# Performance work log

Measured on AMD Instinct MI355X. Metric: run time of the kernel, lower is better.

## Reference

```python
import jax, jax.numpy as jnp
import numpy as np
from jax import lax

B0, H0, W0, C0, NH0 = 8, 128, 128, 192, 6
SPLIT = (8, 16)
BN_EPS = 1e-5


def setup_inputs() -> dict:
    key = jax.random.key(0)
    ks = jax.random.split(key, 32)
    r = lambda i, shape, s=0.02: jax.random.normal(ks[i], shape, dtype=jnp.float32) * s
    C, C8 = C0, C0 // 8
    L = H0 * W0
    return dict(
        x=jax.random.normal(ks[0], (B0, L, C), dtype=jnp.float32),
        w_qkv=r(1, (C, 3 * C)), b_qkv=r(2, (3 * C,)),
        w_dw1=r(3, (C, 1, 3, 3), 0.1), b_dw1=r(4, (C,)),
        g_bn1=1.0 + r(5, (C,)), be_bn1=r(6, (C,)),
        w_si1=r(7, (C8, C), 0.05), b_si1=r(8, (C8,)),
        g_si=1.0 + r(9, (C8,)), be_si=r(10, (C8,)),
        w_si2=r(11, (1, C8), 0.05), b_si2=r(12, (1,)),
        w_ci1=r(13, (C8, C), 0.05), b_ci1=r(14, (C8,)),
        g_ci=1.0 + r(15, (C8,)), be_ci=r(16, (C8,)),
        w_ci2=r(17, (C, C8), 0.05), b_ci2=r(18, (C,)),
        w_dw2=r(19, (C, 1, 3, 3), 0.1), b_dw2=r(20, (C,)),
        g_bn2=1.0 + r(21, (C,)), be_bn2=r(22, (C,)),
        w_proj=r(23, (C, C)), b_proj=r(24, (C,)),
        H=H0, W=W0,
    )


def _bn(x, g, b):  # eval-mode BatchNorm2d, running_mean=0, running_var=1, NCHW
    return x * (g / jnp.sqrt(1.0 + BN_EPS))[:, None, None] + b[:, None, None]


def _gelu(x):
    return jax.nn.gelu(x, approximate=False)  # torch nn.GELU default (erf)


def _dwconv3x3(x, w, b):  # x:(B,C,H,W), w:(C,1,3,3) depthwise
    y = lax.conv_general_dilated(x, w, (1, 1), 'SAME',
                                 feature_group_count=x.shape[1],
                                 dimension_numbers=('NCHW', 'OIHW', 'NCHW'))
    return y + b[:, None, None]


def _c1x1(x, w, b):  # 1x1 conv, w:(O,C)
    return jnp.einsum('bchw,oc->bohw', x, w) + b[:, None, None]


def _win_attn(q, k, v, H, W, Hs, Ws, nh):
    # q,k,v: (B, H*W, Cb). qkv1==qkv2==qkv3 in the source (same Linear on same x),
    # so attn1+attn2+attn3 == 3*attn1 and v1+v2+v3 == 3*v1 (faithful math).
    B, L, Cb = q.shape
    hd = Cb // nh
    scale = hd ** (-0.5)
    T = Hs * Ws

    def to_win(t):  # (B,L,Cb) -> (nW, nh, T, hd)
        t = t.reshape(B, H // Hs, Hs, W // Ws, Ws, Cb)
        t = t.transpose(0, 1, 3, 2, 4, 5).reshape(-1, T, nh, hd)
        return t.transpose(0, 2, 1, 3)

    qw, kw, vw = to_win(q), to_win(k), to_win(v)
    attn = jnp.einsum('wntd,wnsd->wnts', qw, kw) * (3.0 * scale)
    attn = jax.nn.softmax(attn, axis=-1)
    out = jnp.einsum('wnts,wnsd->wntd', attn, 3.0 * vw)  # (nW, nh, T, hd)
    out = out.transpose(0, 2, 1, 3).reshape(-1, T, Cb)
    out = out.reshape(B, H // Hs, W // Ws, Hs, Ws, Cb)
    out = out.transpose(0, 1, 3, 2, 4, 5).reshape(B, H, W, Cb)
    return out


def _forward(x, w_qkv, b_qkv, w_dw1, b_dw1, g_bn1, be_bn1,
             w_si1, b_si1, g_si, be_si, w_si2, b_si2,
             w_ci1, b_ci1, g_ci, be_ci, w_ci2, b_ci2,
             w_dw2, b_dw2, g_bn2, be_bn2, w_proj, b_proj, H, W):
    B, L, C = x.shape
    Ch = C // 2
    nh = NH0 // 2

    qkv = (x @ w_qkv + b_qkv).reshape(B, L, 3, C).transpose(2, 0, 1, 3)  # (3,B,L,C)
    mx = max(SPLIT)
    pad_b = (mx - H % mx) % mx
    pad_r = (mx - W % mx) % mx
    qi = qkv.reshape(3 * B, H, W, C)
    qi = jnp.pad(qi, ((0, 0), (0, pad_b), (0, pad_r), (0, 0)))
    _H, _W = H + pad_b, W + pad_r
    qkv = qi.reshape(3, B, _H * _W, C)
    q, k, v = qkv[0], qkv[1], qkv[2]

    fu1 = _win_attn(q[..., :Ch], k[..., :Ch], v[..., :Ch], _H, _W, SPLIT[0], SPLIT[1], nh)
    fu2 = _win_attn(q[..., Ch:], k[..., Ch:], v[..., Ch:], _H, _W, SPLIT[1], SPLIT[0], nh)
    fu = jnp.concatenate([fu1[:, :H, :W, :].reshape(B, L, Ch),
                          fu2[:, :H, :W, :].reshape(B, L, Ch)], axis=-1)

    # NOTE: the source does x.reshape(B,C,L) (a raw reshape, NOT a transpose) -- replicated.
    x_img = x.reshape(B, C, H, W)
    conv_x1 = _gelu(_bn(_dwconv3x3(x_img, w_dw1, b_dw1), g_bn1, be_bn1))

    s = _c1x1(conv_x1, w_si1, b_si1)
    s = _c1x1(_gelu(_bn(s, g_si, be_si)), w_si2, b_si2)   # (B,1,H,W)
    spatial_map = s.reshape(B, L, 1)

    c = conv_x1.mean(axis=(2, 3), keepdims=True)           # AdaptiveAvgPool2d(1)
    c = _c1x1(c, w_ci1, b_ci1)
    c = _c1x1(_gelu(_bn(c, g_ci, be_ci)), w_ci2, b_ci2)    # (B,C,1,1)
    channel_map = c.reshape(B, 1, C)

    fu = fu + fu * jax.nn.sigmoid(spatial_map)
    fu_img = jnp.swapaxes(fu, -2, -1).reshape(B, C, H, W)
    fu_img = _gelu(_bn(_dwconv3x3(fu_img, w_dw2, b_dw2), g_bn2, be_bn2))
    fu = fu_img.transpose(0, 2, 3, 1).reshape(B, L, C)
    fu = fu + fu * jax.nn.sigmoid(channel_map)
    return fu @ w_proj + b_proj


def reference(x, w_qkv, b_qkv, w_dw1, b_dw1, g_bn1, be_bn1,
              w_si1, b_si1, g_si, be_si, w_si2, b_si2,
              w_ci1, b_ci1, g_ci, be_ci, w_ci2, b_ci2,
              w_dw2, b_dw2, g_bn2, be_bn2, w_proj, b_proj, H, W):
    return _forward(x, w_qkv, b_qkv, w_dw1, b_dw1, g_bn1, be_bn1,
                    w_si1, b_si1, g_si, be_si, w_si2, b_si2,
                    w_ci1, b_ci1, g_ci, be_ci, w_ci2, b_ci2,
                    w_dw2, b_dw2, g_bn2, be_bn2, w_proj, b_proj, H, W)
```

## Files before the change

kernel.cpp:

```cpp
#include <hip/hip_runtime.h>

#define Bn 8
#define Hn 128
#define Wn 128
#define Cn 192
#define Ln (Hn*Wn)
#define Mn (Bn*Ln)
#define FUn ((size_t)Mn*Cn)
#define BANKn ((size_t)Mn*96)
#define BN_RSQ 0.9999950000374997f

typedef unsigned short ushort_t;
typedef __attribute__((ext_vector_type(8))) short short8;
typedef __attribute__((ext_vector_type(4))) float f32x4;
typedef __attribute__((ext_vector_type(4))) unsigned int uint4v;

static __device__ __forceinline__ float gelu_f(float x) {
    return 0.5f * x * (1.0f + erff(x * 0.7071067811865475f));
}
static __device__ __forceinline__ float gate1p(float x) {
    return 1.0f + 1.0f / (1.0f + __expf(-x));
}
static __device__ __forceinline__ unsigned short f2bf(float f) {
    unsigned u = __float_as_uint(f);
    return (unsigned short)((u + 0x7FFFu + ((u >> 16) & 1u)) >> 16);
}
static __device__ __forceinline__ unsigned int pk2(float lo, float hi) {
    return (unsigned int)f2bf(lo) | ((unsigned int)f2bf(hi) << 16);
}
static __device__ __forceinline__ float bf2f(ushort_t u) {
    return __uint_as_float((unsigned)u << 16);
}

__global__ __launch_bounds__(256) void qkv_mfma(const ushort_t* __restrict__ Ab,
        const ushort_t* __restrict__ BwT, const float* __restrict__ bias,
        ushort_t* __restrict__ Qp, ushort_t* __restrict__ Kp,
        ushort_t* __restrict__ Vp)
{
    __shared__ __align__(16) ushort_t smem[128 * 64 + 96 * 64];
    ushort_t* As = smem;
    ushort_t* Bs = smem + 128 * 64;
    ushort_t* St = smem;
    ushort_t* Stv = smem;
    const int g1d = blockIdx.x;
    const int rem = g1d % 48;
    const int sib = rem >> 3;
    const int w8 = rem & 7;
    const int wid = (g1d / 48) * 8 + w8;
    const int br = sib & 1;
    const int partp = sib >> 1;
    const int b = wid >> 7, win = wid & 127;
    const int n0g = partp * 192 + br * 96;
    ushort_t* dst = partp == 0 ? Qp : (partp == 1 ? Kp : Vp);
    ushort_t* bptr = dst + (br ? BANKn : 0);
    int hb, wb;
    if (br == 0) { hb = (win >> 3) * 8;  wb = (win & 7) * 16; }
    else         { hb = (win >> 4) * 16; wb = (win & 15) * 8; }
    const int tid = threadIdx.x;
    const int lane = tid & 63;
    const int wrow = (tid >> 6) * 32;
    const int r0 = lane >> 4, cl = lane & 15;
    f32x4 acc[2][6] = {};

    for (int ks = 0; ks < 3; ++ks) {
        const int k0 = ks * 64;
        if (ks) __syncthreads();
        #pragma unroll
        for (int i = 0; i < 2; ++i) {
            int s = tid + i * 256;
            int row = s >> 2, q = s & 3;
            int l = (br == 0) ? (hb + (row >> 4)) * Wn + wb + (row & 15)
                              : (hb + (row >> 3)) * Wn + wb + (row & 7);
            const ushort_t* src = Ab + (size_t)(b * Ln + l) * 192 + k0 + q * 16;
            uint4 u0 = *(const uint4*)(src);
            uint4 u1 = *(const uint4*)(src + 8);
            int r7 = row & 7;
            *(uint4*)&As[row * 64 + (((q * 2) ^ r7) * 8)] = u0;
            *(uint4*)&As[row * 64 + (((q * 2 + 1) ^ r7) * 8)] = u1;
        }
        #pragma unroll
        for (int i = 0; i < 3; ++i) {
            int f = tid + i * 256;
            int col = f % 96, kslot = f / 96;
            uint4 wv = *(const uint4*)(BwT + (size_t)(n0g + col) * 192 + k0 + kslot * 8);
            *(uint4*)&Bs[col * 64 + ((kslot ^ (col & 7)) * 8)] = wv;
        }
        __syncthreads();
        #pragma unroll
        for (int kk = 0; kk < 2; ++kk) {
            int kslot = kk * 4 + r0;
            int ra0 = wrow + cl, ra1 = wrow + 16 + cl;
            short8 a0 = *(const short8*)&As[ra0 * 64 + ((kslot ^ (ra0 & 7)) * 8)];
            short8 a1 = *(const short8*)&As[ra1 * 64 + ((kslot ^ (ra1 & 7)) * 8)];
            #pragma unroll
            for (int n = 0; n < 6; ++n) {
                int col = n * 16 + cl;
                short8 bn = *(const short8*)&Bs[col * 64 + ((kslot ^ (col & 7)) * 8)];
                acc[0][n] = __builtin_amdgcn_mfma_f32_16x16x32_bf16(a0, bn, acc[0][n], 0, 0, 0);
                acc[1][n] = __builtin_amdgcn_mfma_f32_16x16x32_bf16(a1, bn, acc[1][n], 0, 0, 0);
            }
        }
    }
    float bv[6];
    #pragma unroll
    for (int n = 0; n < 6; ++n) bv[n] = bias[n0g + n * 16 + cl];
    __syncthreads();
    const size_t hbase = (size_t)wid * 3;
    if (partp < 2) {
        #pragma unroll
        for (int m = 0; m < 2; ++m)
            #pragma unroll
            for (int n = 0; n < 6; ++n)
                #pragma unroll
                for (int j = 0; j < 4; ++j) {
                    int t = wrow + m * 16 + r0 * 4 + j;
                    St[t * 104 + n * 16 + cl] = f2bf(acc[m][n][j] + bv[n]);
                }
        __syncthreads();
        #pragma unroll
        for (int i = 0; i < 6; ++i) {
            int f = tid + i * 256;
            int ch8 = f & 3, t = (f >> 2) & 127, hd = f >> 9;
            uint4 v = *(const uint4*)&St[t * 104 + hd * 32 + ch8 * 8];
            *(uint4*)(bptr + (hbase + hd) * 4096 + t * 32 + ch8 * 8) = v;
        }
    } else {
        #pragma unroll
        for (int m = 0; m < 2; ++m)
            #pragma unroll
            for (int n = 0; n < 6; ++n)
                #pragma unroll
                for (int j = 0; j < 4; ++j) {
                    int t = wrow + m * 16 + r0 * 4 + j;
                    Stv[(n * 16 + cl) * 136 + t] = f2bf(acc[m][n][j] + bv[n]);
                }
        __syncthreads();
        #pragma unroll
        for (int i = 0; i < 6; ++i) {
            int f = tid + i * 256;
            int t16 = f & 15, ch = (f >> 4) & 31, hd = f >> 9;
            uint4 v = *(const uint4*)&Stv[(hd * 32 + ch) * 136 + t16 * 8];
            *(uint4*)(bptr + (hbase + hd) * 4096 + ch * 128 + t16 * 8) = v;
        }
    }
}

__global__ __launch_bounds__(256) void proj_mfma(const ushort_t* __restrict__ Ab,
        const ushort_t* __restrict__ BwT, const float* __restrict__ bias,
        float* __restrict__ Cout)
{
    __shared__ __align__(16) ushort_t As[128 * 64];
    __shared__ __align__(16) ushort_t Bs[96 * 64];
    const int m0 = blockIdx.x * 128;
    const int n0 = blockIdx.y * 96;
    const int tid = threadIdx.x;
    const int lane = tid & 63;
    const int wrow = (tid >> 6) * 32;
    const int r0 = lane >> 4, cl = lane & 15;
    f32x4 acc[2][6] = {};

    for (int ks = 0; ks < 3; ++ks) {
        const int k0 = ks * 64;
        if (ks) __syncthreads();
        #pragma unroll
        for (int i = 0; i < 2; ++i) {
            int s = tid + i * 256;
            int row = s >> 2, q = s & 3;
            const ushort_t* src = Ab + (size_t)(m0 + row) * 192 + k0 + q * 16;
            uint4 u0 = *(const uint4*)(src);
            uint4 u1 = *(const uint4*)(src + 8);
            int r7 = row & 7;
            *(uint4*)&As[row * 64 + (((q * 2) ^ r7) * 8)] = u0;
            *(uint4*)&As[row * 64 + (((q * 2 + 1) ^ r7) * 8)] = u1;
        }
        #pragma unroll
        for (int i = 0; i < 3; ++i) {
            int f = tid + i * 256;
            int col = f % 96, kslot = f / 96;
            uint4 wv = *(const uint4*)(BwT + (size_t)(n0 + col) * 192 + k0 + kslot * 8);
            *(uint4*)&Bs[col * 64 + ((kslot ^ (col & 7)) * 8)] = wv;
        }
        __syncthreads();
        #pragma unroll
        for (int kk = 0; kk < 2; ++kk) {
            int kslot = kk * 4 + r0;
            int ra0 = wrow + cl, ra1 = wrow + 16 + cl;
            short8 a0 = *(const short8*)&As[ra0 * 64 + ((kslot ^ (ra0 & 7)) * 8)];
            short8 a1 = *(const short8*)&As[ra1 * 64 + ((kslot ^ (ra1 & 7)) * 8)];
            #pragma unroll
            for (int n = 0; n < 6; ++n) {
                int col = n * 16 + cl;
                short8 bn = *(const short8*)&Bs[col * 64 + ((kslot ^ (col & 7)) * 8)];
                acc[0][n] = __builtin_amdgcn_mfma_f32_16x16x32_bf16(a0, bn, acc[0][n], 0, 0, 0);
                acc[1][n] = __builtin_amdgcn_mfma_f32_16x16x32_bf16(a1, bn, acc[1][n], 0, 0, 0);
            }
        }
    }
    #pragma unroll
    for (int m = 0; m < 2; ++m) {
        #pragma unroll
        for (int n = 0; n < 6; ++n) {
            int col = n0 + n * 16 + cl;
            float bv = bias[col];
            #pragma unroll
            for (int j = 0; j < 4; ++j) {
                int row = m0 + wrow + m * 16 + r0 * 4 + j;
                Cout[(size_t)row * 192 + col] = acc[m][n][j] + bv;
            }
        }
    }
}

__global__ __launch_bounds__(256) void attn_mfma(const ushort_t* __restrict__ Qp,
        const ushort_t* __restrict__ Kp, const ushort_t* __restrict__ Vp,
        const float* __restrict__ gate_s, ushort_t* __restrict__ fu_b)
{
    const int widx = threadIdx.x >> 6;
    const int idx = blockIdx.x * 4 + widx;
    const int jhalf = idx & 1;
    const int sub0 = idx >> 1;
    const int branch = (sub0 >= 3072) ? 1 : 0;
    const int sub = sub0 - branch * 3072;
    const int head = sub >> 10;
    const int b = (sub >> 7) & 7;
    const int win = sub & 127;
    const int L = threadIdx.x & 63;
    const int g = L >> 4, q = L & 15;
    int hb, wb;
    if (branch == 0) { hb = (win >> 3) * 8;  wb = (win & 7) * 16; }
    else             { hb = (win >> 4) * 16; wb = (win & 15) * 8; }
    const int cf = branch * 96 + head * 32;
    const int jbase = jhalf * 4;

    const size_t base = (branch ? BANKn : 0)
                      + ((size_t)(b * 128 + win) * 3 + head) * 4096;
    const ushort_t* Qw = Qp + base;
    const ushort_t* Kw = Kp + base;
    const ushort_t* Vw = Vp + base;

    short8 kf[8], qf[4];
    #pragma unroll
    for (int i = 0; i < 8; ++i)
        kf[i] = *(const short8*)(Kw + (16 * i + q) * 32 + 8 * g);
    #pragma unroll
    for (int jj = 0; jj < 4; ++jj)
        qf[jj] = *(const short8*)(Qw + (16 * (jbase + jj) + q) * 32 + 8 * g);
    short8 vf[2][4];
    #pragma unroll
    for (int dblk = 0; dblk < 2; ++dblk)
        #pragma unroll
        for (int s = 0; s < 4; ++s)
            vf[dblk][s] = *(const short8*)(Vw + (16 * dblk + q) * 128 + 32 * s + 8 * g);

    const float SC = 0.5303300858899106f;
    const int src0 = q + ((g & 1) << 5);
    const bool thi = (g >> 1) != 0;
    const bool glo = (g < 2);
    #pragma unroll
    for (int jj = 0; jj < 4; ++jj) {
        const int j = jbase + jj;
        unsigned wA[8], wB[8];
        float ss = 0.0f;
        #pragma unroll
        for (int i = 0; i < 8; ++i) {
            f32x4 z = {};
            f32x4 S = __builtin_amdgcn_mfma_f32_16x16x32_bf16(kf[i], qf[jj], z, 0, 0, 0);
            float p0 = __expf(S[0] * SC), p1 = __expf(S[1] * SC);
            float p2 = __expf(S[2] * SC), p3 = __expf(S[3] * SC);
            ss += (p0 + p1) + (p2 + p3);
            wA[i] = pk2(p0, p1);
            wB[i] = pk2(p2, p3);
        }
        ss += __shfl_xor(ss, 16);
        ss += __shfl_xor(ss, 32);
        int l_own;
        if (branch == 0) l_own = (hb + j) * Wn + wb + q;
        else             l_own = (hb + 2 * j + (q >> 3)) * Wn + wb + (q & 7);
        float s_own = 3.0f * gate_s[(size_t)b * Ln + l_own] / ss;

        f32x4 O0 = {}, O1 = {};
        #pragma unroll
        for (int s = 0; s < 4; ++s) {
            unsigned a0  = (unsigned)__shfl((int)wA[2*s],     src0);
            unsigned b0  = (unsigned)__shfl((int)wB[2*s],     src0);
            unsigned a0h = (unsigned)__shfl((int)wA[2*s],     src0 + 16);
            unsigned b0h = (unsigned)__shfl((int)wB[2*s],     src0 + 16);
            unsigned a1  = (unsigned)__shfl((int)wA[2*s+1],   src0);
            unsigned b1  = (unsigned)__shfl((int)wB[2*s+1],   src0);
            unsigned a1h = (unsigned)__shfl((int)wA[2*s+1],   src0 + 16);
            unsigned b1h = (unsigned)__shfl((int)wB[2*s+1],   src0 + 16);
            uint4v B2u;
            B2u[0] = thi ? a1  : a0;
            B2u[1] = thi ? b1  : b0;
            B2u[2] = thi ? a1h : a0h;
            B2u[3] = thi ? b1h : b0h;
            short8 B2 = *(short8*)&B2u;
            O0 = __builtin_amdgcn_mfma_f32_16x16x32_bf16(vf[0][s], B2, O0, 0, 0, 0);
            O1 = __builtin_amdgcn_mfma_f32_16x16x32_bf16(vf[1][s], B2, O1, 0, 0, 0);
        }
        unsigned w0 = pk2(O0[0] * s_own, O0[1] * s_own);
        unsigned w1 = pk2(O0[2] * s_own, O0[3] * s_own);
        unsigned w2 = pk2(O1[0] * s_own, O1[1] * s_own);
        unsigned w3 = pk2(O1[2] * s_own, O1[3] * s_own);
        unsigned a0 = (unsigned)__shfl((int)w0, src0);
        unsigned a1 = (unsigned)__shfl((int)w1, src0);
        unsigned b0 = (unsigned)__shfl((int)w0, src0 + 16);
        unsigned b1 = (unsigned)__shfl((int)w1, src0 + 16);
        unsigned c0 = (unsigned)__shfl((int)w2, src0);
        unsigned c1 = (unsigned)__shfl((int)w3, src0);
        unsigned d0 = (unsigned)__shfl((int)w2, src0 + 16);
        unsigned d1 = (unsigned)__shfl((int)w3, src0 + 16);
        uint4 o = make_uint4(glo ? a0 : c0, glo ? a1 : c1,
                             glo ? b0 : d0, glo ? b1 : d1);
        *(uint4*)(fu_b + (size_t)(b * Ln + l_own) * 192 + cf + 8 * g) = o;
    }
}

__global__ __launch_bounds__(256) void conv1_k(const float* __restrict__ x,
        const float* __restrict__ wdw, const float* __restrict__ bdw,
        const float* __restrict__ g1, const float* __restrict__ be1,
        const float* __restrict__ w_qkv, const float* __restrict__ w_proj,
        ushort_t* __restrict__ conv1b, ushort_t* __restrict__ xb,
        ushort_t* __restrict__ wqkvT, ushort_t* __restrict__ wprojT,
        float* __restrict__ pooled16)
{
    if (blockIdx.y == 0) {
        int gid = blockIdx.x * 256 + threadIdx.x;
        if (gid < 192 * 576) {
            int k = gid / 576, n = gid - k * 576;
            wqkvT[(size_t)n * 192 + k] = f2bf(w_qkv[gid]);
        } else if (gid < 192 * 576 + 192 * 192) {
            int g2 = gid - 192 * 576;
            int k = g2 / 192, n = g2 - k * 192;
            wprojT[(size_t)n * 192 + k] = f2bf(w_proj[g2]);
        }
    }
    int bc = blockIdx.x;
    int rg = blockIdx.y;
    int c = bc % 192;
    const float* plane = x + (size_t)bc * Ln;
    int t = threadIdx.x;
    int sx = t & 31, sy = t >> 5;
    int w0 = sx * 4, h = rg * 8 + sy;
    float wk[9];
    #pragma unroll
    for (int i = 0; i < 9; ++i) wk[i] = wdw[c * 9 + i];
    float gb = g1[c] * BN_RSQ, bb = be1[c], bd = bdw[c];

    float a[3][6];
    #pragma unroll
    for (int i = 0; i < 3; ++i) {
        int hh = h - 1 + i;
        float4 m = make_float4(0.f, 0.f, 0.f, 0.f);
        if (hh >= 0 && hh < Hn)
            m = *(const float4*)(plane + hh * Wn + w0);
        float lf = __shfl_up(m.w, 1);
        float rt = __shfl_down(m.x, 1);
        a[i][0] = sx ? lf : 0.0f;
        a[i][1] = m.x; a[i][2] = m.y; a[i][3] = m.z; a[i][4] = m.w;
        a[i][5] = (sx < 31) ? rt : 0.0f;
    }
    *(uint2*)(xb + (size_t)bc * Ln + h * Wn + w0) =
        make_uint2(pk2(a[1][1], a[1][2]), pk2(a[1][3], a[1][4]));
    float psum = 0.0f;
    float o[4];
    #pragma unroll
    for (int p = 0; p < 4; ++p) {
        float s = wk[0] * a[0][p];
        s = fmaf(wk[1], a[0][p + 1], s);
        s = fmaf(wk[2], a[0][p + 2], s);
        s = fmaf(wk[3], a[1][p],     s);
        s = fmaf(wk[4], a[1][p + 1], s);
        s = fmaf(wk[5], a[1][p + 2], s);
        s = fmaf(wk[6], a[2][p],     s);
        s = fmaf(wk[7], a[2][p + 1], s);
        s = fmaf(wk[8], a[2][p + 2], s);
        float y = gelu_f((s + bd) * gb + bb);
        psum += y;
        o[p] = y;
    }
    *(uint2*)(conv1b + (size_t)bc * Ln + h * Wn + w0) =
        make_uint2(pk2(o[0], o[1]), pk2(o[2], o[3]));
    __shared__ float red[4];
    for (int off = 32; off; off >>= 1) psum += __shfl_down(psum, off);
    if ((t & 63) == 0) red[t >> 6] = psum;
    __syncthreads();
    if (t == 0)
        pooled16[bc * 16 + rg] = red[0] + red[1] + red[2] + red[3];
}

__global__ __launch_bounds__(192) void gates_k(const ushort_t* __restrict__ conv1b,
        const float* __restrict__ pooled16,
        const float* __restrict__ ws1g, const float* __restrict__ bs1,
        const float* __restrict__ gsi, const float* __restrict__ besi,
        const float* __restrict__ ws2, const float* __restrict__ bs2,
        const float* __restrict__ w1, const float* __restrict__ b1,
        const float* __restrict__ gci, const float* __restrict__ beci,
        const float* __restrict__ w2, const float* __restrict__ b2,
        float* __restrict__ gate_s, float* __restrict__ gate_c)
{
    int blk = blockIdx.x;
    int tid = threadIdx.x;
    if (blk < Bn * Hn) {
        int b = blk >> 7, h = blk & 127;
        __shared__ float ws1T[192 * 24];
        for (int i = tid; i < 192 * 24; i += 192) {
            int c = i / 24, o = i - c * 24;
            ws1T[i] = ws1g[o * 192 + c];
        }
        __syncthreads();
        if (tid < 128) {
            int w = tid;
            float acc24[24] = {};
            const ushort_t* base = conv1b + (size_t)b * 192 * Ln + h * Wn + w;
            #pragma unroll 4
            for (int c = 0; c < 192; ++c) {
                float v = bf2f(base[(size_t)c * Ln]);
                const float4* wp = (const float4*)&ws1T[c * 24];
                #pragma unroll
                for (int o4 = 0; o4 < 6; ++o4) {
                    float4 wv = wp[o4];
                    acc24[o4*4+0] = fmaf(v, wv.x, acc24[o4*4+0]);
                    acc24[o4*4+1] = fmaf(v, wv.y, acc24[o4*4+1]);
                    acc24[o4*4+2] = fmaf(v, wv.z, acc24[o4*4+2]);
                    acc24[o4*4+3] = fmaf(v, wv.w, acc24[o4*4+3]);
                }
            }
            float s2 = bs2[0];
            #pragma unroll
            for (int o = 0; o < 24; ++o)
                s2 = fmaf(gelu_f((acc24[o] + bs1[o]) * (gsi[o] * BN_RSQ) + besi[o]),
                          ws2[o], s2);
            gate_s[(size_t)blk * 128 + w] = gate1p(s2);
        }
    } else {
        int b = blk - Bn * Hn;
        __shared__ float pl[192];
        __shared__ float h1[24];
        int bc = b * 192 + tid;
        float s = 0.0f;
        #pragma unroll
        for (int i = 0; i < 16; ++i) s += pooled16[bc * 16 + i];
        pl[tid] = s * (1.0f / Ln);
        __syncthreads();
        if (tid < 24) {
            float a = b1[tid];
            for (int c = 0; c < 192; ++c) a = fmaf(pl[c], w1[tid * 192 + c], a);
            a = a * (gci[tid] * BN_RSQ) + beci[tid];
            h1[tid] = gelu_f(a);
        }
        __syncthreads();
        float a = b2[tid];
        #pragma unroll
        for (int o = 0; o < 24; ++o) a = fmaf(h1[o], w2[tid * 24 + o], a);
        gate_c[b * 192 + tid] = gate1p(a);
    }
}

__global__ __launch_bounds__(256) void dwconv2_k(const ushort_t* __restrict__ fu_b,
        const float* __restrict__ gate_c,
        const float* __restrict__ wdw, const float* __restrict__ bdw,
        const float* __restrict__ g2, const float* __restrict__ be2,
        ushort_t* __restrict__ out2b)
{
    int bh = blockIdx.x >> 1;
    int whalf = blockIdx.x & 1;
    int b = bh >> 7, h = bh & 127;
    int tid = threadIdx.x;
    __shared__ float cwp[24 * 105];
    for (int idx = tid; idx < 24 * 96; idx += 256) {
        int c8 = idx / 96, r = idx - c8 * 96;
        float v;
        if (r < 72) {
            int i = r / 9, p = r - i * 9;
            v = wdw[(c8 * 8 + i) * 9 + p];
        } else {
            int r2 = r - 72;
            int i = r2 / 3, j = r2 - i * 3;
            int c = c8 * 8 + i;
            float A = g2[c] * BN_RSQ;
            v = (j == 0) ? A : (j == 1) ? fmaf(bdw[c], A, be2[c])
                                        : gate_c[b * 192 + c];
        }
        cwp[c8 * 105 + r] = v;
    }
    __syncthreads();
    const size_t outrow = (size_t)(b * Ln + h * Wn) * 192;
    for (int it = 0; it < 6; ++it) {
        int item = it * 256 + tid;
        int w = whalf * 64 + item / 24;
        int c8 = item % 24;
        int co = c8 * 8;
        const float* wp = &cwp[c8 * 105];
        uint4 nb[3][3];
        #pragma unroll
        for (int r = 0; r < 3; ++r)
            #pragma unroll
            for (int d = 0; d < 3; ++d)
                nb[r][d] = make_uint4(0u, 0u, 0u, 0u);
        #pragma unroll
        for (int r = 0; r < 3; ++r) {
            int hh = h - 1 + r;
            if (hh < 0 || hh >= Hn) continue;
            const ushort_t* rp = fu_b + (size_t)(b * Ln + hh * Wn) * 192 + co;
            #pragma unroll
            for (int d = 0; d < 3; ++d) {
                int w2 = w - 1 + d;
                if (w2 < 0 || w2 >= Wn) continue;
                nb[r][d] = *(const uint4*)(rp + (size_t)w2 * 192);
            }
        }
        unsigned ou[4];
        #pragma unroll
        for (int i = 0; i < 8; ++i) {
            float s = 0.0f;
            #pragma unroll
            for (int r = 0; r < 3; ++r) {
                #pragma unroll
                for (int d = 0; d < 3; ++d) {
                    unsigned word = ((const unsigned*)&nb[r][d])[i >> 1];
                    float v = __uint_as_float((i & 1) ? (word & 0xffff0000u)
                                                      : (word << 16));
                    s = fmaf(wp[i * 9 + r * 3 + d], v, s);
                }
            }
            float A = wp[72 + i * 3];
            float Bc = wp[72 + i * 3 + 1];
            float G = wp[72 + i * 3 + 2];
            float y = gelu_f(fmaf(s, A, Bc)) * G;
            if (i & 1) ou[i >> 1] |= (unsigned)f2bf(y) << 16;
            else       ou[i >> 1] = (unsigned)f2bf(y);
        }
        *(uint4*)(out2b + outrow + (size_t)w * 192 + co) =
            make_uint4(ou[0], ou[1], ou[2], ou[3]);
    }
}

extern "C" void kernel_launch(void* const* d_in, const int* in_sizes, int n_in,
                              void* d_out, int out_size, void* d_ws, size_t ws_size,
                              hipStream_t stream) {
    (void)in_sizes; (void)n_in; (void)out_size; (void)ws_size;
    const float* x      = (const float*)d_in[0];
    const float* w_qkv  = (const float*)d_in[1];
    const float* b_qkv  = (const float*)d_in[2];
    const float* w_dw1  = (const float*)d_in[3];
    const float* b_dw1  = (const float*)d_in[4];
    const float* g_bn1  = (const float*)d_in[5];
    const float* be_bn1 = (const float*)d_in[6];
    const float* w_si1  = (const float*)d_in[7];
    const float* b_si1  = (const float*)d_in[8];
    const float* g_si   = (const float*)d_in[9];
    const float* be_si  = (const float*)d_in[10];
    const float* w_si2  = (const float*)d_in[11];
    const float* b_si2  = (const float*)d_in[12];
    const float* w_ci1  = (const float*)d_in[13];
    const float* b_ci1  = (const float*)d_in[14];
    const float* g_ci   = (const float*)d_in[15];
    const float* be_ci  = (const float*)d_in[16];
    const float* w_ci2  = (const float*)d_in[17];
    const float* b_ci2  = (const float*)d_in[18];
    const float* w_dw2  = (const float*)d_in[19];
    const float* b_dw2  = (const float*)d_in[20];
    const float* g_bn2  = (const float*)d_in[21];
    const float* be_bn2 = (const float*)d_in[22];
    const float* w_proj = (const float*)d_in[23];
    const float* b_proj = (const float*)d_in[24];

    float* ws = (float*)d_ws;
    ushort_t* conv1b = (ushort_t*)ws;
    ushort_t* Qp     = (ushort_t*)ws;
    ushort_t* Kp     = (ushort_t*)(ws + FUn / 2);
    ushort_t* out2b  = (ushort_t*)(ws + 8000000);
    float* gate_s    = ws + FUn;
    float* gate_c    = gate_s + (size_t)Bn * Ln;
    float* pooled16  = gate_c + Bn * 192;
    ushort_t* wqkvT  = (ushort_t*)(pooled16 + Bn * 192 * 16);
    ushort_t* wprojT = wqkvT + 576 * 192;
    ushort_t* xb     = (ushort_t*)d_out;
    ushort_t* fu_b   = (ushort_t*)d_out;
    ushort_t* Vp     = (ushort_t*)d_out + FUn;

    conv1_k<<<dim3(Bn * 192, 16), 256, 0, stream>>>(x, w_dw1, b_dw1, g_bn1, be_bn1,
                                                    w_qkv, w_proj,
                                                    conv1b, xb, wqkvT, wprojT, pooled16);
    gates_k<<<Bn * Hn + Bn, 192, 0, stream>>>(conv1b, pooled16,
                                              w_si1, b_si1, g_si, be_si, w_si2, b_si2,
                                              w_ci1, b_ci1, g_ci, be_ci, w_ci2, b_ci2,
                                              gate_s, gate_c);
    qkv_mfma<<<6144, 256, 0, stream>>>(xb, wqkvT, b_qkv, Qp, Kp, Vp);
    attn_mfma<<<3072, 256, 0, stream>>>(Qp, Kp, Vp, gate_s, fu_b);
    dwconv2_k<<<Bn * Hn * 2, 256, 0, stream>>>(fu_b, gate_c,
                                               w_dw2, b_dw2, g_bn2, be_bn2, out2b);
    proj_mfma<<<dim3(Mn / 128, 2), 256, 0, stream>>>(out2b, wprojT, b_proj, (float*)d_out);
}
```

Baseline: 280.7 us.

## Fuse QKV projection with window attention, keeping Q/K/V in shared memory

Each block now computes Q, K and V for one (window, head, branch) by selecting the matching 32-column slices of the QKV weights. It then runs the window attention directly from shared memory instead of writing Q/K/V to global buffers and reading them back in a separate kernel. This removes the global round trip of the QKV intermediates and one kernel launch. The cost is that attention is now spread over 4 warps covering 2 query blocks each, and the workspace layout changes so fu_b lives in ws and is no longer aliased with d_out.

```diff
diff --git a/kernel.cpp b/kernel.cpp
--- a/kernel.cpp
+++ b/kernel.cpp
@@ -7,7 +7,6 @@
 #define Ln (Hn*Wn)
 #define Mn (Bn*Ln)
 #define FUn ((size_t)Mn*Cn)
-#define BANKn ((size_t)Mn*96)
 #define BN_RSQ 0.9999950000374997f
 
 typedef unsigned short ushort_t;
@@ -32,33 +31,31 @@
     return __uint_as_float((unsigned)u << 16);
 }
 
-__global__ __launch_bounds__(256) void qkv_mfma(const ushort_t* __restrict__ Ab,
+__global__ __launch_bounds__(256) void qkvattn_mfma(const ushort_t* __restrict__ Ab,
         const ushort_t* __restrict__ BwT, const float* __restrict__ bias,
-        ushort_t* __restrict__ Qp, ushort_t* __restrict__ Kp,
-        ushort_t* __restrict__ Vp)
+        const float* __restrict__ gate_s, ushort_t* __restrict__ fu_b)
 {
     __shared__ __align__(16) ushort_t smem[128 * 64 + 96 * 64];
     ushort_t* As = smem;
     ushort_t* Bs = smem + 128 * 64;
-    ushort_t* St = smem;
-    ushort_t* Stv = smem;
+    ushort_t* Qlds = smem;
+    ushort_t* Klds = smem + 5120;
+    ushort_t* Vlds = smem + 10240;
     const int g1d = blockIdx.x;
     const int rem = g1d % 48;
     const int sib = rem >> 3;
     const int w8 = rem & 7;
     const int wid = (g1d / 48) * 8 + w8;
     const int br = sib & 1;
-    const int partp = sib >> 1;
+    const int head = sib >> 1;
     const int b = wid >> 7, win = wid & 127;
-    const int n0g = partp * 192 + br * 96;
-    ushort_t* dst = partp == 0 ? Qp : (partp == 1 ? Kp : Vp);
-    ushort_t* bptr = dst + (br ? BANKn : 0);
     int hb, wb;
     if (br == 0) { hb = (win >> 3) * 8;  wb = (win & 7) * 16; }
     else         { hb = (win >> 4) * 16; wb = (win & 15) * 8; }
     const int tid = threadIdx.x;
     const int lane = tid & 63;
-    const int wrow = (tid >> 6) * 32;
+    const int widx = tid >> 6;
+    const int wrow = widx * 32;
     const int r0 = lane >> 4, cl = lane & 15;
     f32x4 acc[2][6] = {};
 
@@ -82,7 +79,9 @@
         for (int i = 0; i < 3; ++i) {
             int f = tid + i * 256;
             int col = f % 96, kslot = f / 96;
-            uint4 wv = *(const uint4*)(BwT + (size_t)(n0g + col) * 192 + k0 + kslot * 8);
+            int part = col >> 5, ch = col & 31;
+            int gcol = part * 192 + br * 96 + head * 32 + ch;
+            uint4 wv = *(const uint4*)(BwT + (size_t)gcol * 192 + k0 + kslot * 8);
             *(uint4*)&Bs[col * 64 + ((kslot ^ (col & 7)) * 8)] = wv;
         }
         __syncthreads();
@@ -103,162 +102,52 @@
     }
     float bv[6];
     #pragma unroll
-    for (int n = 0; n < 6; ++n) bv[n] = bias[n0g + n * 16 + cl];
+    for (int n = 0; n < 6; ++n) {
+        int col = n * 16 + cl;
+        int part = col >> 5, ch = col & 31;
+        bv[n] = bias[part * 192 + br * 96 + head * 32 + ch];
+    }
     __syncthreads();
-    const size_t hbase = (size_t)wid * 3;
-    if (partp < 2) {
-        #pragma unroll
-        for (int m = 0; m < 2; ++m)
-            #pragma unroll
-            for (int n = 0; n < 6; ++n)
-                #pragma unroll
-                for (int j = 0; j < 4; ++j) {
-                    int t = wrow + m * 16 + r0 * 4 + j;
-                    St[t * 104 + n * 16 + cl] = f2bf(acc[m][n][j] + bv[n]);
-                }
-        __syncthreads();
-        #pragma unroll
-        for (int i = 0; i < 6; ++i) {
-            int f = tid + i * 256;
-            int ch8 = f & 3, t = (f >> 2) & 127, hd = f >> 9;
-            uint4 v = *(const uint4*)&St[t * 104 + hd * 32 + ch8 * 8];
-            *(uint4*)(bptr + (hbase + hd) * 4096 + t * 32 + ch8 * 8) = v;
-        }
-    } else {
-        #pragma unroll
-        for (int m = 0; m < 2; ++m)
-            #pragma unroll
-            for (int n = 0; n < 6; ++n)
-                #pragma unroll
-                for (int j = 0; j < 4; ++j) {
-                    int t = wrow + m * 16 + r0 * 4 + j;
-                    Stv[(n * 16 + cl) * 136 + t] = f2bf(acc[m][n][j] + bv[n]);
-                }
-        __syncthreads();
-        #pragma unroll
-        for (int i = 0; i < 6; ++i) {
-            int f = tid + i * 256;
-            int t16 = f & 15, ch = (f >> 4) & 31, hd = f >> 9;
-            uint4 v = *(const uint4*)&Stv[(hd * 32 + ch) * 136 + t16 * 8];
-            *(uint4*)(bptr + (hbase + hd) * 4096 + ch * 128 + t16 * 8) = v;
-        }
-    }
-}
-
-__global__ __launch_bounds__(256) void proj_mfma(const ushort_t* __restrict__ Ab,
-        const ushort_t* __restrict__ BwT, const float* __restrict__ bias,
-        float* __restrict__ Cout)
-{
-    __shared__ __align__(16) ushort_t As[128 * 64];
-    __shared__ __align__(16) ushort_t Bs[96 * 64];
-    const int m0 = blockIdx.x * 128;
-    const int n0 = blockIdx.y * 96;
-    const int tid = threadIdx.x;
-    const int lane = tid & 63;
-    const int wrow = (tid >> 6) * 32;
-    const int r0 = lane >> 4, cl = lane & 15;
-    f32x4 acc[2][6] = {};
-
-    for (int ks = 0; ks < 3; ++ks) {
-        const int k0 = ks * 64;
-        if (ks) __syncthreads();
-        #pragma unroll
-        for (int i = 0; i < 2; ++i) {
-            int s = tid + i * 256;
-            int row = s >> 2, q = s & 3;
-            const ushort_t* src = Ab + (size_t)(m0 + row) * 192 + k0 + q * 16;
-            uint4 u0 = *(const uint4*)(src);
-            uint4 u1 = *(const uint4*)(src + 8);
-            int r7 = row & 7;
-            *(uint4*)&As[row * 64 + (((q * 2) ^ r7) * 8)] = u0;
-            *(uint4*)&As[row * 64 + (((q * 2 + 1) ^ r7) * 8)] = u1;
-        }
-        #pragma unroll
-        for (int i = 0; i < 3; ++i) {
-            int f = tid + i * 256;
-            int col = f % 96, kslot = f / 96;
-            uint4 wv = *(const uint4*)(BwT + (size_t)(n0 + col) * 192 + k0 + kslot * 8);
-            *(uint4*)&Bs[col * 64 + ((kslot ^ (col & 7)) * 8)] = wv;
-        }
-        __syncthreads();
-        #pragma unroll
-        for (int kk = 0; kk < 2; ++kk) {
-            int kslot = kk * 4 + r0;
-            int ra0 = wrow + cl, ra1 = wrow + 16 + cl;
-            short8 a0 = *(const short8*)&As[ra0 * 64 + ((kslot ^ (ra0 & 7)) * 8)];
-            short8 a1 = *(const short8*)&As[ra1 * 64 + ((kslot ^ (ra1 & 7)) * 8)];
-            #pragma unroll
-            for (int n = 0; n < 6; ++n) {
-                int col = n * 16 + cl;
-                short8 bn = *(const short8*)&Bs[col * 64 + ((kslot ^ (col & 7)) * 8)];
-                acc[0][n] = __builtin_amdgcn_mfma_f32_16x16x32_bf16(a0, bn, acc[0][n], 0, 0, 0);
-                acc[1][n] = __builtin_amdgcn_mfma_f32_16x16x32_bf16(a1, bn, acc[1][n], 0, 0, 0);
-            }
-        }
-    }
-    #pragma unroll
-    for (int m = 0; m < 2; ++m) {
+    #pragma unroll
+    for (int m = 0; m < 2; ++m)
         #pragma unroll
         for (int n = 0; n < 6; ++n) {
-            int col = n0 + n * 16 + cl;
-            float bv = bias[col];
+            int part = n >> 1;
+            int ch = (n & 1) * 16 + cl;
             #pragma unroll
             for (int j = 0; j < 4; ++j) {
-                int row = m0 + wrow + m * 16 + r0 * 4 + j;
-                Cout[(size_t)row * 192 + col] = acc[m][n][j] + bv;
-            }
-        }
-    }
-}
-
-__global__ __launch_bounds__(256) void attn_mfma(const ushort_t* __restrict__ Qp,
-        const ushort_t* __restrict__ Kp, const ushort_t* __restrict__ Vp,
-        const float* __restrict__ gate_s, ushort_t* __restrict__ fu_b)
-{
-    const int widx = threadIdx.x >> 6;
-    const int idx = blockIdx.x * 4 + widx;
-    const int jhalf = idx & 1;
-    const int sub0 = idx >> 1;
-    const int branch = (sub0 >= 3072) ? 1 : 0;
-    const int sub = sub0 - branch * 3072;
-    const int head = sub >> 10;
-    const int b = (sub >> 7) & 7;
-    const int win = sub & 127;
-    const int L = threadIdx.x & 63;
-    const int g = L >> 4, q = L & 15;
-    int hb, wb;
-    if (branch == 0) { hb = (win >> 3) * 8;  wb = (win & 7) * 16; }
-    else             { hb = (win >> 4) * 16; wb = (win & 15) * 8; }
-    const int cf = branch * 96 + head * 32;
-    const int jbase = jhalf * 4;
-
-    const size_t base = (branch ? BANKn : 0)
-                      + ((size_t)(b * 128 + win) * 3 + head) * 4096;
-    const ushort_t* Qw = Qp + base;
-    const ushort_t* Kw = Kp + base;
-    const ushort_t* Vw = Vp + base;
-
-    short8 kf[8], qf[4];
+                int t = wrow + m * 16 + r0 * 4 + j;
+                ushort_t val = f2bf(acc[m][n][j] + bv[n]);
+                if (part == 0)      Qlds[t * 40 + ch] = val;
+                else if (part == 1) Klds[t * 40 + ch] = val;
+                else                Vlds[ch * 136 + t] = val;
+            }
+        }
+    __syncthreads();
+
+    const int q = cl, g = r0;
+    short8 kf[8], qf[2];
     #pragma unroll
     for (int i = 0; i < 8; ++i)
-        kf[i] = *(const short8*)(Kw + (16 * i + q) * 32 + 8 * g);
-    #pragma unroll
-    for (int jj = 0; jj < 4; ++jj)
-        qf[jj] = *(const short8*)(Qw + (16 * (jbase + jj) + q) * 32 + 8 * g);
+        kf[i] = *(const short8*)&Klds[(16 * i + q) * 40 + 8 * g];
+    #pragma unroll
+    for (int jj = 0; jj < 2; ++jj)
+        qf[jj] = *(const short8*)&Qlds[(16 * (widx * 2 + jj) + q) * 40 + 8 * g];
     short8 vf[2][4];
     #pragma unroll
     for (int dblk = 0; dblk < 2; ++dblk)
         #pragma unroll
         for (int s = 0; s < 4; ++s)
-            vf[dblk][s] = *(const short8*)(Vw + (16 * dblk + q) * 128 + 32 * s + 8 * g);
+            vf[dblk][s] = *(const short8*)&Vlds[(16 * dblk + q) * 136 + 32 * s + 8 * g];
 
     const float SC = 0.5303300858899106f;
+    const int cf = br * 96 + head * 32;
     const int src0 = q + ((g & 1) << 5);
     const bool thi = (g >> 1) != 0;
     const bool glo = (g < 2);
     #pragma unroll
-    for (int jj = 0; jj < 4; ++jj) {
-        const int j = jbase + jj;
+    for (int jj = 0; jj < 2; ++jj) {
+        const int j = widx * 2 + jj;
         unsigned wA[8], wB[8];
         float ss = 0.0f;
         #pragma unroll
@@ -274,8 +163,8 @@
         ss += __shfl_xor(ss, 16);
         ss += __shfl_xor(ss, 32);
         int l_own;
-        if (branch == 0) l_own = (hb + j) * Wn + wb + q;
-        else             l_own = (hb + 2 * j + (q >> 3)) * Wn + wb + (q & 7);
+        if (br == 0) l_own = (hb + j) * Wn + wb + q;
+        else         l_own = (hb + 2 * j + (q >> 3)) * Wn + wb + (q & 7);
         float s_own = 3.0f * gate_s[(size_t)b * Ln + l_own] / ss;
 
         f32x4 O0 = {}, O1 = {};
@@ -313,6 +202,72 @@
         uint4 o = make_uint4(glo ? a0 : c0, glo ? a1 : c1,
                              glo ? b0 : d0, glo ? b1 : d1);
         *(uint4*)(fu_b + (size_t)(b * Ln + l_own) * 192 + cf + 8 * g) = o;
+    }
+}
+
+__global__ __launch_bounds__(256) void proj_mfma(const ushort_t* __restrict__ Ab,
+        const ushort_t* __restrict__ BwT, const float* __restrict__ bias,
+        float* __restrict__ Cout)
+{
+    __shared__ __align__(16) ushort_t As[128 * 64];
+    __shared__ __align__(16) ushort_t Bs[96 * 64];
+    const int m0 = blockIdx.x * 128;
+    const int n0 = blockIdx.y * 96;
+    const int tid = threadIdx.x;
+    const int lane = tid & 63;
+    const int wrow = (tid >> 6) * 32;
+    const int r0 = lane >> 4, cl = lane & 15;
+    f32x4 acc[2][6] = {};
+
+    for (int ks = 0; ks < 3; ++ks) {
+        const int k0 = ks * 64;
+        if (ks) __syncthreads();
+        #pragma unroll
+        for (int i = 0; i < 2; ++i) {
+            int s = tid + i * 256;
+            int row = s >> 2, q = s & 3;
+            const ushort_t* src = Ab + (size_t)(m0 + row) * 192 + k0 + q * 16;
+            uint4 u0 = *(const uint4*)(src);
+            uint4 u1 = *(const uint4*)(src + 8);
+            int r7 = row & 7;
+            *(uint4*)&As[row * 64 + (((q * 2) ^ r7) * 8)] = u0;
+            *(uint4*)&As[row * 64 + (((q * 2 + 1) ^ r7) * 8)] = u1;
+        }
+        #pragma unroll
+        for (int i = 0; i < 3; ++i) {
+            int f = tid + i * 256;
+            int col = f % 96, kslot = f / 96;
+            uint4 wv = *(const uint4*)(BwT + (size_t)(n0 + col) * 192 + k0 + kslot * 8);
+            *(uint4*)&Bs[col * 64 + ((kslot ^ (col & 7)) * 8)] = wv;
+        }
+        __syncthreads();
+        #pragma unroll
+        for (int kk = 0; kk < 2; ++kk) {
+            int kslot = kk * 4 + r0;
+            int ra0 = wrow + cl, ra1 = wrow + 16 + cl;
+            short8 a0 = *(const short8*)&As[ra0 * 64 + ((kslot ^ (ra0 & 7)) * 8)];
+            short8 a1 = *(const short8*)&As[ra1 * 64 + ((kslot ^ (ra1 & 7)) * 8)];
+            #pragma unroll
+            for (int n = 0; n < 6; ++n) {
+                int col = n * 16 + cl;
+                short8 bn = *(const short8*)&Bs[col * 64 + ((kslot ^ (col & 7)) * 8)];
+                acc[0][n] = __builtin_amdgcn_mfma_f32_16x16x32_bf16(a0, bn, acc[0][n], 0, 0, 0);
+                acc[1][n] = __builtin_amdgcn_mfma_f32_16x16x32_bf16(a1, bn, acc[1][n], 0, 0, 0);
+            }
+        }
+    }
+    #pragma unroll
+    for (int m = 0; m < 2; ++m) {
+        #pragma unroll
+        for (int n = 0; n < 6; ++n) {
+            int col = n0 + n * 16 + cl;
+            float bv = bias[col];
+            #pragma unroll
+            for (int j = 0; j < 4; ++j) {
+                int row = m0 + wrow + m * 16 + r0 * 4 + j;
+                Cout[(size_t)row * 192 + col] = acc[m][n][j] + bv;
+            }
+        }
     }
 }
 
@@ -568,17 +523,14 @@
 
     float* ws = (float*)d_ws;
     ushort_t* conv1b = (ushort_t*)ws;
-    ushort_t* Qp     = (ushort_t*)ws;
-    ushort_t* Kp     = (ushort_t*)(ws + FUn / 2);
-    ushort_t* out2b  = (ushort_t*)(ws + 8000000);
+    ushort_t* fu_b   = (ushort_t*)ws;
+    ushort_t* out2b  = (ushort_t*)(ws + FUn / 2);
     float* gate_s    = ws + FUn;
     float* gate_c    = gate_s + (size_t)Bn * Ln;
     float* pooled16  = gate_c + Bn * 192;
     ushort_t* wqkvT  = (ushort_t*)(pooled16 + Bn * 192 * 16);
     ushort_t* wprojT = wqkvT + 576 * 192;
     ushort_t* xb     = (ushort_t*)d_out;
-    ushort_t* fu_b   = (ushort_t*)d_out;
-    ushort_t* Vp     = (ushort_t*)d_out + FUn;
 
     conv1_k<<<dim3(Bn * 192, 16), 256, 0, stream>>>(x, w_dw1, b_dw1, g_bn1, be_bn1,
                                                     w_qkv, w_proj,
@@ -587,8 +539,7 @@
                                               w_si1, b_si1, g_si, be_si, w_si2, b_si2,
                                               w_ci1, b_ci1, g_ci, be_ci, w_ci2, b_ci2,
                                               gate_s, gate_c);
-    qkv_mfma<<<6144, 256, 0, stream>>>(xb, wqkvT, b_qkv, Qp, Kp, Vp);
-    attn_mfma<<<3072, 256, 0, stream>>>(Qp, Kp, Vp, gate_s, fu_b);
+    qkvattn_mfma<<<6144, 256, 0, stream>>>(xb, wqkvT, b_qkv, gate_s, fu_b);
     dwconv2_k<<<Bn * Hn * 2, 256, 0, stream>>>(fu_b, gate_c,
                                                w_dw2, b_dw2, g_bn2, be_bn2, out2b);
     proj_mfma<<<dim3(Mn / 128, 2), 256, 0, stream>>>(out2b, wprojT, b_proj, (float*)d_out);
```

Measured after the change: 280.4 us. No clear change (-0.1%).
